# Kernel tuning notes

Measured on AMD Instinct MI355X. Metric: run time of the kernel, lower is better.

The kernel has to match this reference:

```python
import jax, jax.numpy as jnp
import numpy as np

EPS = 0.0  # torch code divides by norms directly (no eps); inputs are randn so norms > 0


def setup_inputs() -> dict:
    key = jax.random.key(0)
    ks = jax.random.split(key, 16)
    B, C, H, W = 16, 64, 128, 128
    DIM = 4 * C  # 256
    f32 = jnp.float32
    inp = {
        "low": jax.random.normal(ks[0], (B, C, H, W), f32),
        "high": jax.random.normal(ks[1], (B, C, H, W), f32),
        "flow": jax.random.normal(ks[2], (B, C, H, W), f32),
        "feedback": jax.random.normal(ks[3], (B, C, H, W), f32),
        # GCN(4, 64, 64): single graph-conv layer, relu(adj @ x @ W + b)
        "Wgcn": jax.random.normal(ks[4], (C, C), f32) * 0.05,
        "bgcn": jnp.zeros((C,), f32),
        # four SE fc heads: Linear(DIM -> C) + sigmoid
        "W1": jax.random.normal(ks[5], (C, DIM), f32) * 0.05,
        "b1": jnp.zeros((C,), f32),
        "W2": jax.random.normal(ks[6], (C, DIM), f32) * 0.05,
        "b2": jnp.zeros((C,), f32),
        "W3": jax.random.normal(ks[7], (C, DIM), f32) * 0.05,
        "b3": jnp.zeros((C,), f32),
        "W4": jax.random.normal(ks[8], (C, DIM), f32) * 0.05,
        "b4": jnp.zeros((C,), f32),
        # gate: 1x1 Conv2d(DIM -> 64) stored as dense [64, DIM]
        "Wgate": jax.random.normal(ks[9], (C, DIM), f32) * 0.05,
        "bgate": jnp.zeros((C,), f32),
    }
    return inp


def reference(low, high, flow, feedback, Wgcn, bgcn, W1, b1, W2, b2, W3, b3, W4, b4, Wgate, bgate):
    B, C, H, W = low.shape
    # adaptive avg pool(1) of concat([low,high,flow,feedback], dim=1) then view(B,4,C)
    combined_fc = jnp.stack([
        low.mean(axis=(2, 3)),
        high.mean(axis=(2, 3)),
        flow.mean(axis=(2, 3)),
        feedback.mean(axis=(2, 3)),
    ], axis=1)  # [B, 4, C]
    # cosine-similarity adjacency  [B, 4, 4]
    norm = jnp.linalg.norm(combined_fc, axis=2, keepdims=True)  # [B,4,1]
    mul = jnp.einsum('bic,bjc->bij', combined_fc, combined_fc)
    batch_adj = mul / (norm * norm.transpose(0, 2, 1))
    # tiny GCN: relu(adj @ x @ W + b)  -> feat_cat = flatten over nodes
    h = jax.nn.relu(jnp.einsum('bij,bjc,cd->bid', batch_adj, combined_fc, Wgcn) + bgcn)  # [B,4,C]
    feat_cat = h.reshape(B, 4 * C)  # [B, 256]
    sig = jax.nn.sigmoid
    e1 = sig(feat_cat @ W1.T + b1)[:, :, None, None]  # [B,C,1,1]
    e2 = sig(feat_cat @ W2.T + b2)[:, :, None, None]
    e3 = sig(feat_cat @ W3.T + b3)[:, :, None, None]
    e4 = sig(feat_cat @ W4.T + b4)[:, :, None, None]
    wa = low + e2 * high + e3 * flow + e4 * feedback
    wb = e1 * low + high + e3 * flow + e4 * feedback
    wc = e1 * low + e2 * high + flow + e4 * feedback
    wd = e1 * low + e2 * high + e3 * flow + feedback
    feat = jnp.concatenate([wa, wb, wc, wd], axis=1)  # [B, 4C, H, W]
    # 1x1 conv == channel GEMM
    out = jnp.einsum('bchw,oc->bohw', feat, Wgate) + bgate[None, :, None, None]
    return out
```

## Files before the change

### kernel.cpp

```cpp
#include <hip/hip_runtime.h>
#include <cmath>

#define BB 16
#define CC 64
#define PP 16384

typedef float f32x4 __attribute__((ext_vector_type(4)));
typedef short bf16x8 __attribute__((ext_vector_type(8)));
typedef int i32x4 __attribute__((ext_vector_type(4)));
typedef unsigned int u32;

__device__ __forceinline__ void split_pair(float v0, float v1, u32& hi, u32& lo) {
    u32 u0 = __builtin_bit_cast(u32, v0);
    u32 u1 = __builtin_bit_cast(u32, v1);
    u32 h0 = u0 & 0xFFFF0000u;
    u32 h1 = u1 & 0xFFFF0000u;
    hi = (h0 >> 16) | h1;
    float l0 = v0 - __builtin_bit_cast(float, h0);
    float l1 = v1 - __builtin_bit_cast(float, h1);
    lo = (__builtin_bit_cast(u32, l0) >> 16) | (__builtin_bit_cast(u32, l1) & 0xFFFF0000u);
}

__global__ __launch_bounds__(256) void k_means(const float* __restrict__ low,
                                               const float* __restrict__ high,
                                               const float* __restrict__ flow,
                                               const float* __restrict__ fb,
                                               float* __restrict__ cf) {
    int g0 = blockIdx.x * 2;
    int b = g0 >> 8, t = (g0 >> 6) & 3, c = g0 & 63;
    const float* in = (t == 0) ? low : (t == 1) ? high : (t == 2) ? flow : fb;
    const float4* p = (const float4*)(in + ((size_t)(b * CC + c)) * PP);
    int tid = threadIdx.x;

    float s0 = 0.f, s1 = 0.f;
    #pragma unroll
    for (int i = 0; i < 16; ++i) {
        float4 va = p[tid + i * 256];
        float4 vb = p[4096 + tid + i * 256];
        s0 += (va.x + va.y) + (va.z + va.w);
        s1 += (vb.x + vb.y) + (vb.z + vb.w);
    }
    #pragma unroll
    for (int off = 32; off > 0; off >>= 1) {
        s0 += __shfl_down(s0, off, 64);
        s1 += __shfl_down(s1, off, 64);
    }

    __shared__ float r[2][4];
    if ((tid & 63) == 0) { r[0][tid >> 6] = s0; r[1][tid >> 6] = s1; }
    __syncthreads();
    if (tid == 0) {
        cf[g0]     = ((r[0][0] + r[0][1]) + (r[0][2] + r[0][3])) * (1.0f / PP);
        cf[g0 + 1] = ((r[1][0] + r[1][1]) + (r[1][2] + r[1][3])) * (1.0f / PP);
    }
}

__global__ __launch_bounds__(256) void k_small(const float* __restrict__ cf,
    const float* __restrict__ Wgcn, const float* __restrict__ bgcn,
    const float* __restrict__ W1, const float* __restrict__ b1,
    const float* __restrict__ W2, const float* __restrict__ b2,
    const float* __restrict__ W3, const float* __restrict__ b3,
    const float* __restrict__ W4, const float* __restrict__ b4,
    const float* __restrict__ Wgate,
    u32* __restrict__ Ah, u32* __restrict__ Al) {
    int b = blockIdx.x;
    int tid = threadIdx.x;
    int lane = tid & 63;
    int wid = tid >> 6;
    __shared__ float x[4][64];
    __shared__ float nrm[4];
    __shared__ float adj[16];
    __shared__ float y[4][64];
    __shared__ float fc[256];
    __shared__ float e[4][64];

    x[wid][lane] = cf[b * 256 + tid];
    __syncthreads();

    if (tid < 4) {
        float s = 0.f;
        for (int c = 0; c < 64; ++c) s += x[tid][c] * x[tid][c];
        nrm[tid] = sqrtf(s);
    }
    __syncthreads();

    if (tid < 16) {
        int i = tid >> 2, j = tid & 3;
        float s = 0.f;
        for (int c = 0; c < 64; ++c) s += x[i][c] * x[j][c];
        adj[tid] = s / (nrm[i] * nrm[j]);
    }
    __syncthreads();

    {
        float s = 0.f;
        #pragma unroll
        for (int j = 0; j < 4; ++j) s += adj[wid * 4 + j] * x[j][lane];
        y[wid][lane] = s;
    }
    __syncthreads();

    {
        float s = bgcn[lane];
        for (int c = 0; c < 64; ++c) s += y[wid][c] * Wgcn[c * 64 + lane];
        fc[wid * 64 + lane] = fmaxf(s, 0.f);
    }
    __syncthreads();

    {
        const float* Wk = (wid == 0) ? W1 : (wid == 1) ? W2 : (wid == 2) ? W3 : W4;
        const float* bk = (wid == 0) ? b1 : (wid == 1) ? b2 : (wid == 2) ? b3 : b4;
        float4 fv = *(const float4*)&fc[lane * 4];
        for (int c = 0; c < 64; ++c) {
            float4 w = *(const float4*)(Wk + c * 256 + lane * 4);
            float part = (w.x * fv.x + w.y * fv.y) + (w.z * fv.z + w.w * fv.w);
            #pragma unroll
            for (int off = 32; off > 0; off >>= 1)
                part += __shfl_down(part, off, 64);
            if (lane == 0) {
                float s = part + bk[c];
                e[wid][c] = 1.f / (1.f + expf(-s));
            }
        }
    }
    __syncthreads();

    {
        int t = wid, o = lane;
        const float* wrow = Wgate + o * 256;
        u32* Ahb = Ah + b * 8192;
        u32* Alb = Al + b * 8192;
        #pragma unroll 4
        for (int c4 = 0; c4 < 64; c4 += 4) {
            float4 w0 = *(const float4*)(wrow + c4);
            float4 w1 = *(const float4*)(wrow + 64 + c4);
            float4 w2 = *(const float4*)(wrow + 128 + c4);
            float4 w3 = *(const float4*)(wrow + 192 + c4);
            float4 wt = (t == 0) ? w0 : (t == 1) ? w1 : (t == 2) ? w2 : w3;
            float4 sm = make_float4((w0.x + w1.x) + (w2.x + w3.x),
                                    (w0.y + w1.y) + (w2.y + w3.y),
                                    (w0.z + w1.z) + (w2.z + w3.z),
                                    (w0.w + w1.w) + (w2.w + w3.w));
            float a0 = wt.x + e[t][c4 + 0] * (sm.x - wt.x);
            float a1 = wt.y + e[t][c4 + 1] * (sm.y - wt.y);
            float a2 = wt.z + e[t][c4 + 2] * (sm.z - wt.z);
            float a3 = wt.w + e[t][c4 + 3] * (sm.w - wt.w);
            u32 h01, l01, h23, l23;
            split_pair(a0, a1, h01, l01);
            split_pair(a2, a3, h23, l23);
            int k2 = (t * 64 + c4) >> 1;
            Ahb[(k2 + 0) * 64 + o] = h01;
            Alb[(k2 + 0) * 64 + o] = l01;
            Ahb[(k2 + 1) * 64 + o] = h23;
            Alb[(k2 + 1) * 64 + o] = l23;
        }
    }
}

__global__ __launch_bounds__(256, 2) void k_gemm(const float* __restrict__ low,
    const float* __restrict__ high, const float* __restrict__ flow,
    const float* __restrict__ fb, const u32* __restrict__ Ah,
    const u32* __restrict__ Al,
    const float* __restrict__ bgate, float* __restrict__ out) {
    int blk = blockIdx.x;
    int b = blk >> 6;
    int tile = blk & 63;
    int tid = threadIdx.x;
    int lane = tid & 63;
    int wv = tid >> 6;
    int l15 = lane & 15;
    int kq = (lane >> 4) << 3;

    int pbase = tile * 256 + wv * 64 + l15;
    size_t xoff = (size_t)b * (CC * PP) + (size_t)kq * PP + pbase;
    const float* px[4] = {low + xoff, high + xoff, flow + xoff, fb + xoff};
    const u32* Ahp = Ah + b * 8192 + (kq >> 1) * 64 + l15;
    const u32* Alp = Al + b * 8192 + (kq >> 1) * 64 + l15;

    f32x4 acc[4][4];
    #pragma unroll
    for (int i = 0; i < 4; ++i)
        #pragma unroll
        for (int j = 0; j < 4; ++j) acc[i][j] = (f32x4)(0.f);

    #pragma unroll
    for (int t = 0; t < 4; ++t) {
        const float* xp = px[t];
        #pragma unroll
        for (int h = 0; h < 2; ++h) {
            float xr[4][8];
            #pragma unroll
            for (int pt = 0; pt < 4; ++pt)
                #pragma unroll
                for (int j = 0; j < 8; ++j)
                    xr[pt][j] = xp[(size_t)(h * 32 + j) * PP + pt * 16];

            bf16x8 ah[4], al[4];
            #pragma unroll
            for (int ot = 0; ot < 4; ++ot) {
                i32x4 hv, lv;
                #pragma unroll
                for (int d = 0; d < 4; ++d) {
                    int row = t * 32 + h * 16 + d;
                    hv[d] = (int)Ahp[row * 64 + ot * 16];
                    lv[d] = (int)Alp[row * 64 + ot * 16];
                }
                ah[ot] = __builtin_bit_cast(bf16x8, hv);
                al[ot] = __builtin_bit_cast(bf16x8, lv);
            }

            bf16x8 xh[4], xl[4];
            #pragma unroll
            for (int pt = 0; pt < 4; ++pt) {
                i32x4 hd, ld;
                #pragma unroll
                for (int d = 0; d < 4; ++d) {
                    u32 hi, lo;
                    split_pair(xr[pt][2 * d], xr[pt][2 * d + 1], hi, lo);
                    hd[d] = (int)hi; ld[d] = (int)lo;
                }
                xh[pt] = __builtin_bit_cast(bf16x8, hd);
                xl[pt] = __builtin_bit_cast(bf16x8, ld);
            }

            #pragma unroll
            for (int ot = 0; ot < 4; ++ot)
                #pragma unroll
                for (int pt = 0; pt < 4; ++pt) {
                    acc[ot][pt] = __builtin_amdgcn_mfma_f32_16x16x32_bf16(
                        ah[ot], xh[pt], acc[ot][pt], 0, 0, 0);
                    acc[ot][pt] = __builtin_amdgcn_mfma_f32_16x16x32_bf16(
                        ah[ot], xl[pt], acc[ot][pt], 0, 0, 0);
                    acc[ot][pt] = __builtin_amdgcn_mfma_f32_16x16x32_bf16(
                        al[ot], xh[pt], acc[ot][pt], 0, 0, 0);
                }
        }
    }

    int rg = lane >> 4;
    size_t obase = (size_t)b * (CC * PP) + (size_t)pbase;
    #pragma unroll
    for (int ot = 0; ot < 4; ++ot)
        #pragma unroll
        for (int r = 0; r < 4; ++r) {
            int o = ot * 16 + rg * 4 + r;
            float bg = bgate[o];
            #pragma unroll
            for (int pt = 0; pt < 4; ++pt)
                out[obase + (size_t)o * PP + pt * 16] = acc[ot][pt][r] + bg;
        }
}

extern "C" void kernel_launch(void* const* d_in, const int* in_sizes, int n_in,
                              void* d_out, int out_size, void* d_ws, size_t ws_size,
                              hipStream_t stream) {
    const float* low  = (const float*)d_in[0];
    const float* high = (const float*)d_in[1];
    const float* flow = (const float*)d_in[2];
    const float* fb   = (const float*)d_in[3];
    const float* Wgcn = (const float*)d_in[4];
    const float* bgcn = (const float*)d_in[5];
    const float* W1   = (const float*)d_in[6];
    const float* b1   = (const float*)d_in[7];
    const float* W2   = (const float*)d_in[8];
    const float* b2   = (const float*)d_in[9];
    const float* W3   = (const float*)d_in[10];
    const float* b3   = (const float*)d_in[11];
    const float* W4   = (const float*)d_in[12];
    const float* b4   = (const float*)d_in[13];
    const float* Wgate = (const float*)d_in[14];
    const float* bgate = (const float*)d_in[15];
    float* out = (float*)d_out;

    float* cf = (float*)d_ws;
    u32* Ah   = (u32*)d_ws + 4096;
    u32* Al   = (u32*)d_ws + 4096 + BB * 8192;

    k_means<<<BB * 4 * CC / 2, 256, 0, stream>>>(low, high, flow, fb, cf);
    k_small<<<BB, 256, 0, stream>>>(cf, Wgcn, bgcn, W1, b1, W2, b2, W3, b3,
                                    W4, b4, Wgate, Ah, Al);
    k_gemm<<<BB * CC, 256, 0, stream>>>(low, high, flow, fb, Ah, Al, bgate, out);
}
```

Before: 413.8 us.

## Retune means kernel, stream A-fragment loads, drop occupancy hint, nontemporal output stores

The means kernel now uses one block per channel plane instead of two, loading all 16 float4 values up front before reducing. In the GEMM kernel, the weight fragments are loaded one output tile ahead inside the MFMA loop instead of all at once. This lowers register pressure, and the min-blocks hint of 2 is removed from launch bounds. Output stores become nontemporal to avoid cache pollution. These trade extra grid blocks and a different register and occupancy balance for less live state and better streaming.

```diff
diff --git a/kernel.cpp b/kernel.cpp
--- a/kernel.cpp
+++ b/kernel.cpp
@@ -26,33 +26,28 @@
                                                const float* __restrict__ flow,
                                                const float* __restrict__ fb,
                                                float* __restrict__ cf) {
-    int g0 = blockIdx.x * 2;
-    int b = g0 >> 8, t = (g0 >> 6) & 3, c = g0 & 63;
+    int g = blockIdx.x;
+    int b = g >> 8, t = (g >> 6) & 3, c = g & 63;
     const float* in = (t == 0) ? low : (t == 1) ? high : (t == 2) ? flow : fb;
     const float4* p = (const float4*)(in + ((size_t)(b * CC + c)) * PP);
     int tid = threadIdx.x;
 
-    float s0 = 0.f, s1 = 0.f;
-    #pragma unroll
-    for (int i = 0; i < 16; ++i) {
-        float4 va = p[tid + i * 256];
-        float4 vb = p[4096 + tid + i * 256];
-        s0 += (va.x + va.y) + (va.z + va.w);
-        s1 += (vb.x + vb.y) + (vb.z + vb.w);
-    }
-    #pragma unroll
-    for (int off = 32; off > 0; off >>= 1) {
-        s0 += __shfl_down(s0, off, 64);
-        s1 += __shfl_down(s1, off, 64);
-    }
-
-    __shared__ float r[2][4];
-    if ((tid & 63) == 0) { r[0][tid >> 6] = s0; r[1][tid >> 6] = s1; }
-    __syncthreads();
-    if (tid == 0) {
-        cf[g0]     = ((r[0][0] + r[0][1]) + (r[0][2] + r[0][3])) * (1.0f / PP);
-        cf[g0 + 1] = ((r[1][0] + r[1][1]) + (r[1][2] + r[1][3])) * (1.0f / PP);
-    }
+    float4 v[16];
+    #pragma unroll
+    for (int i = 0; i < 16; ++i) v[i] = p[tid + i * 256];
+
+    float s = 0.f;
+    #pragma unroll
+    for (int i = 0; i < 16; ++i) s += (v[i].x + v[i].y) + (v[i].z + v[i].w);
+
+    #pragma unroll
+    for (int off = 32; off > 0; off >>= 1) s += __shfl_down(s, off, 64);
+
+    __shared__ float r[4];
+    if ((tid & 63) == 0) r[tid >> 6] = s;
+    __syncthreads();
+    if (tid == 0)
+        cf[g] = ((r[0] + r[1]) + (r[2] + r[3])) * (1.0f / PP);
 }
 
 __global__ __launch_bounds__(256) void k_small(const float* __restrict__ cf,
@@ -157,7 +152,7 @@
     }
 }
 
-__global__ __launch_bounds__(256, 2) void k_gemm(const float* __restrict__ low,
+__global__ __launch_bounds__(256) void k_gemm(const float* __restrict__ low,
     const float* __restrict__ high, const float* __restrict__ flow,
     const float* __restrict__ fb, const u32* __restrict__ Ah,
     const u32* __restrict__ Al,
@@ -195,18 +190,12 @@
                 for (int j = 0; j < 8; ++j)
                     xr[pt][j] = xp[(size_t)(h * 32 + j) * PP + pt * 16];
 
-            bf16x8 ah[4], al[4];
-            #pragma unroll
-            for (int ot = 0; ot < 4; ++ot) {
-                i32x4 hv, lv;
-                #pragma unroll
-                for (int d = 0; d < 4; ++d) {
-                    int row = t * 32 + h * 16 + d;
-                    hv[d] = (int)Ahp[row * 64 + ot * 16];
-                    lv[d] = (int)Alp[row * 64 + ot * 16];
-                }
-                ah[ot] = __builtin_bit_cast(bf16x8, hv);
-                al[ot] = __builtin_bit_cast(bf16x8, lv);
+            i32x4 hc, lc;
+            #pragma unroll
+            for (int d = 0; d < 4; ++d) {
+                int row = t * 32 + h * 16 + d;
+                hc[d] = (int)Ahp[row * 64];
+                lc[d] = (int)Alp[row * 64];
             }
 
             bf16x8 xh[4], xl[4];
@@ -224,16 +213,27 @@
             }
 
             #pragma unroll
-            for (int ot = 0; ot < 4; ++ot)
+            for (int ot = 0; ot < 4; ++ot) {
+                bf16x8 ah = __builtin_bit_cast(bf16x8, hc);
+                bf16x8 al = __builtin_bit_cast(bf16x8, lc);
+                if (ot < 3) {
+                    #pragma unroll
+                    for (int d = 0; d < 4; ++d) {
+                        int row = t * 32 + h * 16 + d;
+                        hc[d] = (int)Ahp[row * 64 + (ot + 1) * 16];
+                        lc[d] = (int)Alp[row * 64 + (ot + 1) * 16];
+                    }
+                }
                 #pragma unroll
                 for (int pt = 0; pt < 4; ++pt) {
                     acc[ot][pt] = __builtin_amdgcn_mfma_f32_16x16x32_bf16(
-                        ah[ot], xh[pt], acc[ot][pt], 0, 0, 0);
+                        ah, xh[pt], acc[ot][pt], 0, 0, 0);
                     acc[ot][pt] = __builtin_amdgcn_mfma_f32_16x16x32_bf16(
-                        ah[ot], xl[pt], acc[ot][pt], 0, 0, 0);
+                        ah, xl[pt], acc[ot][pt], 0, 0, 0);
                     acc[ot][pt] = __builtin_amdgcn_mfma_f32_16x16x32_bf16(
-                        al[ot], xh[pt], acc[ot][pt], 0, 0, 0);
+                        al, xh[pt], acc[ot][pt], 0, 0, 0);
                 }
+            }
         }
     }
 
@@ -247,7 +247,8 @@
             float bg = bgate[o];
             #pragma unroll
             for (int pt = 0; pt < 4; ++pt)
-                out[obase + (size_t)o * PP + pt * 16] = acc[ot][pt][r] + bg;
+                __builtin_nontemporal_store(acc[ot][pt][r] + bg,
+                    out + obase + (size_t)o * PP + pt * 16);
         }
 }
 
@@ -276,7 +277,7 @@
     u32* Ah   = (u32*)d_ws + 4096;
     u32* Al   = (u32*)d_ws + 4096 + BB * 8192;
 
-    k_means<<<BB * 4 * CC / 2, 256, 0, stream>>>(low, high, flow, fb, cf);
+    k_means<<<BB * 4 * CC, 256, 0, stream>>>(low, high, flow, fb, cf);
     k_small<<<BB, 256, 0, stream>>>(cf, Wgcn, bgcn, W1, b1, W2, b2, W3, b3,
                                     W4, b4, Wgate, Ah, Al);
     k_gemm<<<BB * CC, 256, 0, stream>>>(low, high, flow, fb, Ah, Al, bgate, out);
```

New measurement: 390.8 us. 5.6% less time.
